# Performance work log

Measured on AMD Instinct MI355X. Metric: run time of the kernel, lower is better.

Reference implementation:

```python
import jax, jax.numpy as jnp
import numpy as np

ROPE_BASE = 10000.0


def _rope_tables(T, d, dtype):
    # inv_freq over even indices, emb = concat(freqs, freqs) -> [T, d]
    inv_freq = 1.0 / (ROPE_BASE ** (jnp.arange(0, d, 2, dtype=jnp.float32) / d))
    t = jnp.arange(T, dtype=jnp.float32)
    freqs = jnp.einsum('i,j->ij', t, inv_freq)          # [T, d/2]
    emb = jnp.concatenate([freqs, freqs], axis=-1)      # [T, d]
    return jnp.cos(emb).astype(dtype), jnp.sin(emb).astype(dtype)


def _rotate_half(x):
    d = x.shape[-1] // 2
    return jnp.concatenate([-x[..., d:], x[..., :d]], axis=-1)


def _apply_rope(x, cos, sin):
    # x: [B, T, H, Dh]; cos/sin: [T, Dh] broadcast over batch and heads
    c = cos[None, :, None, :]
    s = sin[None, :, None, :]
    return x * c + _rotate_half(x) * s


def setup_inputs() -> dict:
    key = jax.random.key(0)
    k1, k2, k3 = jax.random.split(key, 3)
    B, T, C = 2, 2048, 1024
    x = jax.random.normal(k1, (B, T, C), dtype=jnp.float32)
    # weights stored as [in, out] (transposed nn.Linear), scaled like torch init
    W_qkv = jax.random.normal(k2, (C, 3 * C), dtype=jnp.float32) * (C ** -0.5)
    W_proj = jax.random.normal(k3, (C, C), dtype=jnp.float32) * (C ** -0.5)
    return {'x': x, 'W_qkv': W_qkv, 'W_proj': W_proj}


def reference(x, W_qkv, W_proj):
    B, T, C = x.shape
    H = 16
    Dh = C // H
    qkv = x @ W_qkv                                   # [B, T, 3C]
    q, k, v = jnp.split(qkv, 3, axis=-1)
    q = q.reshape(B, T, H, Dh)
    k = k.reshape(B, T, H, Dh)
    v = v.reshape(B, T, H, Dh)
    cos, sin = _rope_tables(T, Dh, x.dtype)
    q = _apply_rope(q, cos, sin)
    k = _apply_rope(k, cos, sin)
    scale = 1.0 / jnp.sqrt(jnp.asarray(Dh, dtype=x.dtype))
    # causal SDPA: scores [B, H, T, T]
    scores = jnp.einsum('bqhd,bkhd->bhqk', q, k) * scale
    causal = jnp.tril(jnp.ones((T, T), dtype=bool))
    scores = jnp.where(causal[None, None], scores, jnp.asarray(-jnp.inf, dtype=scores.dtype))
    attn = jax.nn.softmax(scores, axis=-1)
    y = jnp.einsum('bhqk,bkhd->bqhd', attn, v).reshape(B, T, C)
    return y @ W_proj
```

## Files before the change

kernel.cpp:

```cpp
#include <hip/hip_runtime.h>
#include <cstdint>
#include <cstddef>

typedef __bf16 bf16;
typedef __bf16 bf16x2 __attribute__((ext_vector_type(2)));
typedef __bf16 bf16x4 __attribute__((ext_vector_type(4)));
typedef __bf16 bf16x8 __attribute__((ext_vector_type(8)));
typedef float  f32x4  __attribute__((ext_vector_type(4)));
typedef float  f32x16 __attribute__((ext_vector_type(16)));
typedef int    i32x4  __attribute__((ext_vector_type(4)));

#define G2L(src, dst)                                                          \
  __builtin_amdgcn_global_load_lds(                                            \
      (const __attribute__((address_space(1))) unsigned int*)(src),            \
      (__attribute__((address_space(3))) unsigned int*)(dst), 16, 0, 0)

__global__ void k_f32_to_bf16(const float* __restrict__ in, bf16* __restrict__ out, int n) {
  int i = (blockIdx.x * blockDim.x + threadIdx.x) * 8;
  if (i >= n) return;
  float4 a = *(const float4*)(in + i);
  float4 b = *(const float4*)(in + i + 4);
  bf16x8 o;
  o[0] = (bf16)a.x; o[1] = (bf16)a.y; o[2] = (bf16)a.z; o[3] = (bf16)a.w;
  o[4] = (bf16)b.x; o[5] = (bf16)b.y; o[6] = (bf16)b.z; o[7] = (bf16)b.w;
  *(bf16x8*)(out + i) = o;
}

__global__ void k_transpose_f32_bf16(const float* __restrict__ in, bf16* __restrict__ out,
                                     int R, int C) {
  __shared__ float tile[32][33];
  int c0 = blockIdx.x * 32, r0 = blockIdx.y * 32;
  int tx = threadIdx.x & 31, ty = threadIdx.x >> 5;
#pragma unroll
  for (int i = 0; i < 32; i += 8)
    tile[ty + i][tx] = in[(size_t)(r0 + ty + i) * C + c0 + tx];
  __syncthreads();
#pragma unroll
  for (int i = 0; i < 32; i += 8)
    out[(size_t)(c0 + ty + i) * R + r0 + tx] = (bf16)tile[tx][ty + i];
}

__global__ void k_rope_tables(float* __restrict__ cosT, float* __restrict__ sinT, int total) {
  int i = blockIdx.x * blockDim.x + threadIdx.x;
  if (i >= total) return;
  int t = i >> 5, j = i & 31;
  float inv = powf(10000.0f, -(float)j * (1.0f / 32.0f));
  float f = (float)t * inv;
  cosT[i] = cosf(f);
  sinT[i] = sinf(f);
}

__global__ void k_rope_qk(const bf16* __restrict__ qkv, const float* __restrict__ cosT,
                          const float* __restrict__ sinT, bf16* __restrict__ qr,
                          bf16* __restrict__ kr) {
  int i = blockIdx.x * blockDim.x + threadIdx.x;
  int j = i & 31;
  int h = (i >> 5) & 15;
  int t = (i >> 9) & 2047;
  int b = i >> 20;
  size_t base = (size_t)(b * 2048 + t) * 3072;
  float c = cosT[t * 32 + j], s = sinT[t * 32 + j];
  float qlo = (float)qkv[base + h * 64 + j];
  float qhi = (float)qkv[base + h * 64 + j + 32];
  float klo = (float)qkv[base + 1024 + h * 64 + j];
  float khi = (float)qkv[base + 1024 + h * 64 + j + 32];
  size_t ob = ((size_t)(b * 16 + h) * 2048 + t) * 64;
  qr[ob + j]      = (bf16)((qlo * c - qhi * s) * 0.125f);
  qr[ob + j + 32] = (bf16)((qhi * c + qlo * s) * 0.125f);
  kr[ob + j]      = (bf16)(klo * c - khi * s);
  kr[ob + j + 32] = (bf16)(khi * c + klo * s);
}

__global__ void k_v_scatter(const bf16* __restrict__ qkv, bf16* __restrict__ vt) {
  __shared__ bf16 tile[64][66];
  int bh = blockIdx.y;
  int t0 = blockIdx.x * 64;
  int b = bh >> 4, h = bh & 15;
  int tt = threadIdx.x >> 2, c4 = (threadIdx.x & 3) * 16;
  const bf16* src = qkv + (size_t)(b * 2048 + t0 + tt) * 3072 + 2048 + h * 64 + c4;
  bf16x8 v0 = *(const bf16x8*)src;
  bf16x8 v1 = *(const bf16x8*)(src + 8);
#pragma unroll
  for (int j = 0; j < 8; j++) { tile[tt][c4 + j] = v0[j]; tile[tt][c4 + 8 + j] = v1[j]; }
  __syncthreads();
  int d = threadIdx.x >> 2, tc0 = (threadIdx.x & 3) * 16;
  bf16x8 o0, o1;
#pragma unroll
  for (int j = 0; j < 8; j++) { o0[j] = tile[tc0 + j][d]; o1[j] = tile[tc0 + 8 + j][d]; }
  bf16* dst = vt + ((size_t)bh * 64 + d) * 2048 + t0 + tc0;
  *(bf16x8*)dst = o0;
  *(bf16x8*)(dst + 8) = o1;
}

template <int OUTF32>
__global__ __launch_bounds__(256) void k_gemm_bt(const bf16* __restrict__ A,
                                                 const bf16* __restrict__ Bt,
                                                 float* __restrict__ Cf, bf16* __restrict__ Cb,
                                                 int M, int N, int K) {
  __shared__ __align__(16) bf16 sA[128 * 64];
  __shared__ __align__(16) bf16 sB[128 * 64];
  int m0 = blockIdx.y * 128, n0 = blockIdx.x * 128;
  int t = threadIdx.x, lane = t & 63, w = t >> 6;
  int wr = w >> 1, wc = w & 1;
  int lr = lane & 15, q2 = lane >> 4;
  int srow8 = lane >> 3, pc8 = lane & 7;
  f32x4 acc[4][4] = {};
  for (int k0 = 0; k0 < K; k0 += 64) {
#pragma unroll
    for (int is = 0; is < 4; is++) {
      int r = w * 32 + is * 8 + srow8;
      int lc = pc8 ^ (r & 7);
      G2L(A + (size_t)(m0 + r) * K + k0 + lc * 8, &sA[(w * 32 + is * 8) * 64]);
    }
#pragma unroll
    for (int is = 0; is < 4; is++) {
      int r = w * 32 + is * 8 + srow8;
      int lc = pc8 ^ (r & 7);
      G2L(Bt + (size_t)(n0 + r) * K + k0 + lc * 8, &sB[(w * 32 + is * 8) * 64]);
    }
    __syncthreads();
#pragma unroll
    for (int ch = 0; ch < 2; ch++) {
      bf16x8 af[4], bfr[4];
#pragma unroll
      for (int i = 0; i < 4; i++) {
        int r = wr * 64 + i * 16 + lr;
        af[i] = *(const bf16x8*)&sA[r * 64 + (((ch * 4 + q2) ^ (r & 7)) * 8)];
      }
#pragma unroll
      for (int i = 0; i < 4; i++) {
        int r = wc * 64 + i * 16 + lr;
        bfr[i] = *(const bf16x8*)&sB[r * 64 + (((ch * 4 + q2) ^ (r & 7)) * 8)];
      }
#pragma unroll
      for (int mi = 0; mi < 4; mi++)
#pragma unroll
        for (int ni = 0; ni < 4; ni++)
          acc[mi][ni] = __builtin_amdgcn_mfma_f32_16x16x32_bf16(af[mi], bfr[ni], acc[mi][ni], 0, 0, 0);
    }
    __syncthreads();
  }
  int row_base = m0 + wr * 64, col_base = n0 + wc * 64;
#pragma unroll
  for (int mi = 0; mi < 4; mi++)
#pragma unroll
    for (int ni = 0; ni < 4; ni++) {
      int col = col_base + ni * 16 + lr;
#pragma unroll
      for (int r = 0; r < 4; r++) {
        int row = row_base + mi * 16 + q2 * 4 + r;
        float v = acc[mi][ni][r];
        if (OUTF32) Cf[(size_t)row * N + col] = v;
        else        Cb[(size_t)row * N + col] = (bf16)v;
      }
    }
}

__global__ __launch_bounds__(128) void k_flash(const bf16* __restrict__ qr,
                                               const bf16* __restrict__ kr,
                                               const bf16* __restrict__ vt,
                                               bf16* __restrict__ out) {
  const int T = 2048;
  int id = blockIdx.x;
  int qb = 31 - (id >> 5);
  int bh = id & 31;
  int b = bh >> 4, h = bh & 15;
  __shared__ __align__(16) bf16 sK[2][64 * 64];
  __shared__ __align__(16) bf16 sV[2][64 * 64];
  int t = threadIdx.x, lane = t & 63, w = t >> 6;
  int q31 = lane & 31, hi = lane >> 5;
  int srow8 = lane >> 3, pc8 = lane & 7;

  const bf16* Kbh = kr + (size_t)bh * T * 64;
  const bf16* Vbh = vt + (size_t)bh * 64 * T;

  int nk = qb + 1;
  int qwb = qb * 64 + w * 32;
  int qg = qwb + q31;

  const bf16* qrow = qr + ((size_t)bh * T + qg) * 64 + hi * 8;
  bf16x8 qf[4];
#pragma unroll
  for (int ks = 0; ks < 4; ks++) qf[ks] = *(const bf16x8*)(qrow + ks * 16);
  f32x16 o0 = {}, o1 = {};
  float m = -1e30f, l = 0.f;

  auto stage = [&](int buf, int kt) {
#pragma unroll
    for (int is = 0; is < 4; is++) {
      int r = w * 32 + is * 8 + srow8;
      int lc = pc8 ^ (r & 7);
      G2L(Kbh + (size_t)(kt * 64 + r) * 64 + lc * 8, &sK[buf][(w * 32 + is * 8) * 64]);
    }
#pragma unroll
    for (int is = 0; is < 4; is++) {
      int d = w * 32 + is * 8 + srow8;
      int lc = pc8 ^ (d & 7);
      G2L(Vbh + (size_t)d * T + kt * 64 + lc * 8, &sV[buf][(w * 32 + is * 8) * 64]);
    }
  };

  stage(0, 0);
  for (int kt = 0; kt < nk; kt++) {
    int buf = kt & 1;
    if (kt + 1 < nk) {
      stage(buf ^ 1, kt + 1);
      asm volatile("s_waitcnt vmcnt(8)" ::: "memory");
    } else {
      asm volatile("s_waitcnt vmcnt(0)" ::: "memory");
    }
    __builtin_amdgcn_s_barrier();
    asm volatile("" ::: "memory");
    __builtin_amdgcn_sched_barrier(0);
    const bf16* Kb = &sK[buf][0];
    const bf16* Vb = &sV[buf][0];
    f32x16 s[2];
    __builtin_amdgcn_s_setprio(1);
#pragma unroll
    for (int kb = 0; kb < 2; kb++) {
      f32x16 a = {};
      int krow = kb * 32 + q31;
#pragma unroll
      for (int ks = 0; ks < 4; ks++) {
        int ch = (ks * 2 + hi) ^ (krow & 7);
        bf16x8 kf = *(const bf16x8*)&Kb[krow * 64 + ch * 8];
        a = __builtin_amdgcn_mfma_f32_32x32x16_bf16(kf, qf[ks], a, 0, 0, 0);
      }
      s[kb] = a;
    }
    __builtin_amdgcn_s_setprio(0);
    if (kt == qb) {
      int thr = qg - kt * 64;
#pragma unroll
      for (int kb = 0; kb < 2; kb++)
#pragma unroll
        for (int r = 0; r < 16; r++) {
          int koff = kb * 32 + (r & 3) + 8 * (r >> 2) + 4 * hi;
          if (koff > thr) s[kb][r] = -1e30f;
        }
    }
    float tm[16];
#pragma unroll
    for (int i = 0; i < 16; i++) tm[i] = fmaxf(s[0][i], s[1][i]);
#pragma unroll
    for (int st = 8; st > 0; st >>= 1)
#pragma unroll
      for (int i = 0; i < st; i++) tm[i] = fmaxf(tm[i], tm[i + st]);
    float px = tm[0];
    px = fmaxf(px, __shfl_xor(px, 32, 64));
    float mn = fmaxf(m, px);
    float alpha = __expf(m - mn);
    m = mn;
    float ts[16];
#pragma unroll
    for (int i = 0; i < 16; i++) {
      float p0 = __expf(s[0][i] - m);
      float p1 = __expf(s[1][i] - m);
      s[0][i] = p0;
      s[1][i] = p1;
      ts[i] = p0 + p1;
    }
#pragma unroll
    for (int st = 8; st > 0; st >>= 1)
#pragma unroll
      for (int i = 0; i < st; i++) ts[i] += ts[i + st];
    float rs = ts[0];
    rs += __shfl_xor(rs, 32, 64);
    l = l * alpha + rs;
    int pw[4][4];
#pragma unroll
    for (int kb = 0; kb < 2; kb++) {
      int wd[8];
#pragma unroll
      for (int g = 0; g < 4; g++) {
        bf16x2 a, c;
        a[0] = (bf16)s[kb][4 * g + 0]; a[1] = (bf16)s[kb][4 * g + 1];
        c[0] = (bf16)s[kb][4 * g + 2]; c[1] = (bf16)s[kb][4 * g + 3];
        wd[2 * g]     = __builtin_bit_cast(int, a);
        wd[2 * g + 1] = __builtin_bit_cast(int, c);
      }
      asm volatile("v_permlane32_swap_b32 %0, %1" : "+v"(wd[0]), "+v"(wd[2]));
      asm volatile("v_permlane32_swap_b32 %0, %1" : "+v"(wd[1]), "+v"(wd[3]));
      asm volatile("v_permlane32_swap_b32 %0, %1" : "+v"(wd[4]), "+v"(wd[6]));
      asm volatile("v_permlane32_swap_b32 %0, %1" : "+v"(wd[5]), "+v"(wd[7]));
      pw[2 * kb][0] = wd[0]; pw[2 * kb][1] = wd[1];
      pw[2 * kb][2] = wd[2]; pw[2 * kb][3] = wd[3];
      pw[2 * kb + 1][0] = wd[4]; pw[2 * kb + 1][1] = wd[5];
      pw[2 * kb + 1][2] = wd[6]; pw[2 * kb + 1][3] = wd[7];
    }
#pragma unroll
    for (int r = 0; r < 16; r++) { o0[r] *= alpha; o1[r] *= alpha; }
    __builtin_amdgcn_s_setprio(1);
#pragma unroll
    for (int ks = 0; ks < 4; ks++) {
      i32x4 pv = {pw[ks][0], pw[ks][1], pw[ks][2], pw[ks][3]};
      bf16x8 pb = __builtin_bit_cast(bf16x8, pv);
      {
        int drow = q31;
        int ch = (ks * 2 + hi) ^ (drow & 7);
        bf16x8 vf = *(const bf16x8*)&Vb[drow * 64 + ch * 8];
        o0 = __builtin_amdgcn_mfma_f32_32x32x16_bf16(vf, pb, o0, 0, 0, 0);
      }
      {
        int drow = 32 + q31;
        int ch = (ks * 2 + hi) ^ (drow & 7);
        bf16x8 vf = *(const bf16x8*)&Vb[drow * 64 + ch * 8];
        o1 = __builtin_amdgcn_mfma_f32_32x32x16_bf16(vf, pb, o1, 0, 0, 0);
      }
    }
    __builtin_amdgcn_s_setprio(0);
    asm volatile("" ::: "memory");
    __builtin_amdgcn_s_barrier();
    asm volatile("" ::: "memory");
  }
  float linv = 1.0f / l;
  bf16* orow = out + ((size_t)b * T + qg) * 1024 + h * 64;
#pragma unroll
  for (int g = 0; g < 4; g++) {
    bf16x4 v0, v1;
#pragma unroll
    for (int j = 0; j < 4; j++) {
      v0[j] = (bf16)(o0[4 * g + j] * linv);
      v1[j] = (bf16)(o1[4 * g + j] * linv);
    }
    *(bf16x4*)&orow[8 * g + 4 * hi]      = v0;
    *(bf16x4*)&orow[32 + 8 * g + 4 * hi] = v1;
  }
}

extern "C" void kernel_launch(void* const* d_in, const int* in_sizes, int n_in,
                              void* d_out, int out_size, void* d_ws, size_t ws_size,
                              hipStream_t stream) {
  const float* x     = (const float*)d_in[0];
  const float* Wqkv  = (const float*)d_in[1];
  const float* Wproj = (const float*)d_in[2];
  float* outp = (float*)d_out;
  const int B = 2, T = 2048, C = 1024;
  const int M = B * T;

  char* ws = (char*)d_ws;
  size_t off = 0;
  auto alloc = [&](size_t bytes) {
    void* p = ws + off;
    off += (bytes + 255) & ~(size_t)255;
    return p;
  };
  bf16* xb     = (bf16*)alloc((size_t)M * C * 2);
  bf16* wqkvt  = (bf16*)alloc((size_t)3 * C * C * 2);
  bf16* wprojt = (bf16*)alloc((size_t)C * C * 2);
  float* cosT  = (float*)alloc((size_t)T * 32 * 4);
  float* sinT  = (float*)alloc((size_t)T * 32 * 4);
  bf16* qkv    = (bf16*)alloc((size_t)M * 3 * C * 2);
  bf16* qr     = (bf16*)alloc((size_t)M * C * 2);
  bf16* kr     = (bf16*)alloc((size_t)M * C * 2);
  bf16* vt     = (bf16*)alloc((size_t)M * C * 2);
  bf16* attn   = qkv;

  k_f32_to_bf16<<<dim3(M * C / 8 / 256), dim3(256), 0, stream>>>(x, xb, M * C);
  k_transpose_f32_bf16<<<dim3(3 * C / 32, C / 32), dim3(256), 0, stream>>>(Wqkv, wqkvt, C, 3 * C);
  k_transpose_f32_bf16<<<dim3(C / 32, C / 32), dim3(256), 0, stream>>>(Wproj, wprojt, C, C);
  k_rope_tables<<<dim3(T * 32 / 256), dim3(256), 0, stream>>>(cosT, sinT, T * 32);
  k_gemm_bt<0><<<dim3(3 * C / 128, M / 128), dim3(256), 0, stream>>>(xb, wqkvt, (float*)nullptr, qkv, M, 3 * C, C);
  k_rope_qk<<<dim3((B * T * 16 * 32) / 256), dim3(256), 0, stream>>>(qkv, cosT, sinT, qr, kr);
  k_v_scatter<<<dim3(T / 64, 32), dim3(256), 0, stream>>>(qkv, vt);
  k_flash<<<dim3(1024), dim3(128), 0, stream>>>(qr, kr, vt, attn);
  k_gemm_bt<1><<<dim3(C / 128, M / 128), dim3(256), 0, stream>>>(attn, wprojt, outp, (bf16*)nullptr, M, C, C);
}
```

Before: 140.8 us.

## Split causal flash attention across KV chunks and merge partials in combine kernel

The flash kernel now splits each query tile's causal KV range into chunks of up to 8 key tiles, launching 2560 blocks instead of 1024, so long rows no longer dominate the tail. Each block writes unnormalized bf16 partial outputs plus per-row max and sum, and a new combine kernel rescales and merges them into the attention output. Double-buffered K/V staging is replaced by a single buffer with a full wait, which removes load/compute overlap. The change also adds an extra launch, extra global traffic for the partials, and bf16 rounding of unnormalized partial outputs.

```diff
diff --git a/kernel.cpp b/kernel.cpp
--- a/kernel.cpp
+++ b/kernel.cpp
@@ -156,17 +156,25 @@
     }
 }
 
-__global__ __launch_bounds__(128) void k_flash(const bf16* __restrict__ qr,
-                                               const bf16* __restrict__ kr,
-                                               const bf16* __restrict__ vt,
-                                               bf16* __restrict__ out) {
+__global__ __launch_bounds__(128) void k_flash_part(const bf16* __restrict__ qr,
+                                                    const bf16* __restrict__ kr,
+                                                    const bf16* __restrict__ vt,
+                                                    bf16* __restrict__ Opart,
+                                                    float* __restrict__ ml) {
   const int T = 2048;
   int id = blockIdx.x;
-  int qb = 31 - (id >> 5);
+  int slot = id >> 5;
   int bh = id & 31;
-  int b = bh >> 4, h = bh & 15;
-  __shared__ __align__(16) bf16 sK[2][64 * 64];
-  __shared__ __align__(16) bf16 sV[2][64 * 64];
+  int qt, c;
+  if (slot < 8)       { qt = slot; c = 0; }
+  else if (slot < 24) { int s = slot - 8;  qt = 8 + (s >> 1);  c = s & 1; }
+  else if (slot < 48) { int s = slot - 24; qt = 16 + s / 3;    c = s - (qt - 16) * 3; }
+  else                { int s = slot - 48; qt = 24 + (s >> 2); c = s & 3; }
+  int kt0 = c * 8;
+  int kt1 = qt + 1 < kt0 + 8 ? qt + 1 : kt0 + 8;
+
+  __shared__ __align__(16) bf16 sK[64 * 64];
+  __shared__ __align__(16) bf16 sV[64 * 64];
   int t = threadIdx.x, lane = t & 63, w = t >> 6;
   int q31 = lane & 31, hi = lane >> 5;
   int srow8 = lane >> 3, pc8 = lane & 7;
@@ -174,10 +182,8 @@
   const bf16* Kbh = kr + (size_t)bh * T * 64;
   const bf16* Vbh = vt + (size_t)bh * 64 * T;
 
-  int nk = qb + 1;
-  int qwb = qb * 64 + w * 32;
+  int qwb = qt * 64 + w * 32;
   int qg = qwb + q31;
-
   const bf16* qrow = qr + ((size_t)bh * T + qg) * 64 + hi * 8;
   bf16x8 qf[4];
 #pragma unroll
@@ -185,35 +191,27 @@
   f32x16 o0 = {}, o1 = {};
   float m = -1e30f, l = 0.f;
 
-  auto stage = [&](int buf, int kt) {
+  auto stage = [&](int kt) {
 #pragma unroll
     for (int is = 0; is < 4; is++) {
       int r = w * 32 + is * 8 + srow8;
       int lc = pc8 ^ (r & 7);
-      G2L(Kbh + (size_t)(kt * 64 + r) * 64 + lc * 8, &sK[buf][(w * 32 + is * 8) * 64]);
+      G2L(Kbh + (size_t)(kt * 64 + r) * 64 + lc * 8, &sK[(w * 32 + is * 8) * 64]);
     }
 #pragma unroll
     for (int is = 0; is < 4; is++) {
       int d = w * 32 + is * 8 + srow8;
       int lc = pc8 ^ (d & 7);
-      G2L(Vbh + (size_t)d * T + kt * 64 + lc * 8, &sV[buf][(w * 32 + is * 8) * 64]);
+      G2L(Vbh + (size_t)d * T + kt * 64 + lc * 8, &sV[(w * 32 + is * 8) * 64]);
     }
   };
 
-  stage(0, 0);
-  for (int kt = 0; kt < nk; kt++) {
-    int buf = kt & 1;
-    if (kt + 1 < nk) {
-      stage(buf ^ 1, kt + 1);
-      asm volatile("s_waitcnt vmcnt(8)" ::: "memory");
-    } else {
-      asm volatile("s_waitcnt vmcnt(0)" ::: "memory");
-    }
+  stage(kt0);
+  for (int kt = kt0; kt < kt1; kt++) {
+    asm volatile("s_waitcnt vmcnt(0)" ::: "memory");
     __builtin_amdgcn_s_barrier();
     asm volatile("" ::: "memory");
     __builtin_amdgcn_sched_barrier(0);
-    const bf16* Kb = &sK[buf][0];
-    const bf16* Vb = &sV[buf][0];
     f32x16 s[2];
     __builtin_amdgcn_s_setprio(1);
 #pragma unroll
@@ -223,13 +221,13 @@
 #pragma unroll
       for (int ks = 0; ks < 4; ks++) {
         int ch = (ks * 2 + hi) ^ (krow & 7);
-        bf16x8 kf = *(const bf16x8*)&Kb[krow * 64 + ch * 8];
+        bf16x8 kf = *(const bf16x8*)&sK[krow * 64 + ch * 8];
         a = __builtin_amdgcn_mfma_f32_32x32x16_bf16(kf, qf[ks], a, 0, 0, 0);
       }
       s[kb] = a;
     }
     __builtin_amdgcn_s_setprio(0);
-    if (kt == qb) {
+    if (kt == qt) {
       int thr = qg - kt * 64;
 #pragma unroll
       for (int kb = 0; kb < 2; kb++)
@@ -273,11 +271,11 @@
       int wd[8];
 #pragma unroll
       for (int g = 0; g < 4; g++) {
-        bf16x2 a, c;
+        bf16x2 a, cc;
         a[0] = (bf16)s[kb][4 * g + 0]; a[1] = (bf16)s[kb][4 * g + 1];
-        c[0] = (bf16)s[kb][4 * g + 2]; c[1] = (bf16)s[kb][4 * g + 3];
+        cc[0] = (bf16)s[kb][4 * g + 2]; cc[1] = (bf16)s[kb][4 * g + 3];
         wd[2 * g]     = __builtin_bit_cast(int, a);
-        wd[2 * g + 1] = __builtin_bit_cast(int, c);
+        wd[2 * g + 1] = __builtin_bit_cast(int, cc);
       }
       asm volatile("v_permlane32_swap_b32 %0, %1" : "+v"(wd[0]), "+v"(wd[2]));
       asm volatile("v_permlane32_swap_b32 %0, %1" : "+v"(wd[1]), "+v"(wd[3]));
@@ -298,13 +296,13 @@
       {
         int drow = q31;
         int ch = (ks * 2 + hi) ^ (drow & 7);
-        bf16x8 vf = *(const bf16x8*)&Vb[drow * 64 + ch * 8];
+        bf16x8 vf = *(const bf16x8*)&sV[drow * 64 + ch * 8];
         o0 = __builtin_amdgcn_mfma_f32_32x32x16_bf16(vf, pb, o0, 0, 0, 0);
       }
       {
         int drow = 32 + q31;
         int ch = (ks * 2 + hi) ^ (drow & 7);
-        bf16x8 vf = *(const bf16x8*)&Vb[drow * 64 + ch * 8];
+        bf16x8 vf = *(const bf16x8*)&sV[drow * 64 + ch * 8];
         o1 = __builtin_amdgcn_mfma_f32_32x32x16_bf16(vf, pb, o1, 0, 0, 0);
       }
     }
@@ -312,20 +310,69 @@
     asm volatile("" ::: "memory");
     __builtin_amdgcn_s_barrier();
     asm volatile("" ::: "memory");
-  }
-  float linv = 1.0f / l;
-  bf16* orow = out + ((size_t)b * T + qg) * 1024 + h * 64;
+    if (kt + 1 < kt1) stage(kt + 1);
+  }
+  int qloc = w * 32 + q31;
+  bf16* Ob = Opart + (size_t)id * 4096 + qloc * 64;
 #pragma unroll
   for (int g = 0; g < 4; g++) {
     bf16x4 v0, v1;
 #pragma unroll
     for (int j = 0; j < 4; j++) {
-      v0[j] = (bf16)(o0[4 * g + j] * linv);
-      v1[j] = (bf16)(o1[4 * g + j] * linv);
-    }
-    *(bf16x4*)&orow[8 * g + 4 * hi]      = v0;
-    *(bf16x4*)&orow[32 + 8 * g + 4 * hi] = v1;
-  }
+      v0[j] = (bf16)o0[4 * g + j];
+      v1[j] = (bf16)o1[4 * g + j];
+    }
+    *(bf16x4*)&Ob[8 * g + 4 * hi]      = v0;
+    *(bf16x4*)&Ob[32 + 8 * g + 4 * hi] = v1;
+  }
+  if (hi == 0) {
+    ml[(size_t)id * 128 + qloc]      = m;
+    ml[(size_t)id * 128 + 64 + qloc] = l;
+  }
+}
+
+__global__ __launch_bounds__(256) void k_combine(const bf16* __restrict__ Opart,
+                                                 const float* __restrict__ ml,
+                                                 bf16* __restrict__ attn) {
+  int bhqt = blockIdx.x;
+  int bh = bhqt & 31, qt = bhqt >> 5;
+  int b = bh >> 4, h = bh & 15;
+  int nch = (qt >> 3) + 1;
+  int slot0;
+  if (qt < 8)       slot0 = qt;
+  else if (qt < 16) slot0 = 8 + (qt - 8) * 2;
+  else if (qt < 24) slot0 = 24 + (qt - 16) * 3;
+  else              slot0 = 48 + (qt - 24) * 4;
+  int t = threadIdx.x;
+  int q = t >> 2, ds = (t & 3) * 16;
+  float M = -1e30f;
+  for (int c = 0; c < nch; c++)
+    M = fmaxf(M, ml[(size_t)((slot0 + c) * 32 + bh) * 128 + q]);
+  float acc[16] = {};
+  float L = 0.f;
+  for (int c = 0; c < nch; c++) {
+    int p = (slot0 + c) * 32 + bh;
+    float wgt = __expf(ml[(size_t)p * 128 + q] - M);
+    L += wgt * ml[(size_t)p * 128 + 64 + q];
+    const bf16* row = Opart + (size_t)p * 4096 + q * 64 + ds;
+    bf16x8 a0 = *(const bf16x8*)row;
+    bf16x8 a1 = *(const bf16x8*)(row + 8);
+#pragma unroll
+    for (int i = 0; i < 8; i++) {
+      acc[i]     += wgt * (float)a0[i];
+      acc[i + 8] += wgt * (float)a1[i];
+    }
+  }
+  float Linv = 1.0f / L;
+  bf16x8 w0, w1;
+#pragma unroll
+  for (int i = 0; i < 8; i++) {
+    w0[i] = (bf16)(acc[i] * Linv);
+    w1[i] = (bf16)(acc[i + 8] * Linv);
+  }
+  bf16* dst = attn + ((size_t)(b * 2048) + qt * 64 + q) * 1024 + h * 64 + ds;
+  *(bf16x8*)dst = w0;
+  *(bf16x8*)(dst + 8) = w1;
 }
 
 extern "C" void kernel_launch(void* const* d_in, const int* in_sizes, int n_in,
@@ -354,7 +401,9 @@
   bf16* qr     = (bf16*)alloc((size_t)M * C * 2);
   bf16* kr     = (bf16*)alloc((size_t)M * C * 2);
   bf16* vt     = (bf16*)alloc((size_t)M * C * 2);
-  bf16* attn   = qkv;
+  bf16* attn   = xb;
+  bf16* Opart  = qkv;
+  float* ml    = (float*)(qkv + (size_t)2560 * 4096);
 
   k_f32_to_bf16<<<dim3(M * C / 8 / 256), dim3(256), 0, stream>>>(x, xb, M * C);
   k_transpose_f32_bf16<<<dim3(3 * C / 32, C / 32), dim3(256), 0, stream>>>(Wqkv, wqkvt, C, 3 * C);
@@ -363,6 +412,7 @@
   k_gemm_bt<0><<<dim3(3 * C / 128, M / 128), dim3(256), 0, stream>>>(xb, wqkvt, (float*)nullptr, qkv, M, 3 * C, C);
   k_rope_qk<<<dim3((B * T * 16 * 32) / 256), dim3(256), 0, stream>>>(qkv, cosT, sinT, qr, kr);
   k_v_scatter<<<dim3(T / 64, 32), dim3(256), 0, stream>>>(qkv, vt);
-  k_flash<<<dim3(1024), dim3(128), 0, stream>>>(qr, kr, vt, attn);
+  k_flash_part<<<dim3(2560), dim3(128), 0, stream>>>(qr, kr, vt, Opart, ml);
+  k_combine<<<dim3(1024), dim3(256), 0, stream>>>(Opart, ml, attn);
   k_gemm_bt<1><<<dim3(C / 128, M / 128), dim3(256), 0, stream>>>(attn, wprojt, outp, (bf16*)nullptr, M, C, C);
 }
```

Measured after the change: 136.0 us. -3.4%, faster.
